# Kernel tuning notes

Measured on AMD Instinct MI355X. Metric: run time of the kernel, lower is better.

The kernel has to match this reference:

```python
import jax, jax.numpy as jnp
import numpy as np

H = 8  # num_heads
EPS = 1e-8

def setup_inputs() -> dict:
    key = jax.random.key(0)
    ks = jax.random.split(key, 8)
    B, L, E = 2, 1024, 512
    s = 1.0 / np.sqrt(E)
    return {
        "query": jax.random.normal(ks[0], (B, L, E), jnp.float32),
        "key":   jax.random.normal(ks[1], (B, L, E), jnp.float32),
        "value": jax.random.normal(ks[2], (B, L, E), jnp.float32),
        "Wq": jax.random.normal(ks[3], (E, E), jnp.float32) * s,
        "bq": jnp.zeros((E,), jnp.float32),
        "Wk": jax.random.normal(ks[4], (E, E), jnp.float32) * s,
        "bk": jnp.zeros((E,), jnp.float32),
        "Wv": jax.random.normal(ks[5], (E, E), jnp.float32) * s,
        "bv": jnp.zeros((E,), jnp.float32),
        "Wo": jax.random.normal(ks[6], (E, E), jnp.float32) * s,
        "bo": jnp.zeros((E,), jnp.float32),
    }

def reference(query, key, value, Wq, bq, Wk, bk, Wv, bv, Wo, bo):
    B, Q_len, E = query.shape
    K_len = key.shape[1]
    D = E // H
    q = (query @ Wq.T + bq).reshape(B, Q_len, H, D)
    k = (key   @ Wk.T + bk).reshape(B, K_len, H, D)
    v = (value @ Wv.T + bv).reshape(B, K_len, H, D)
    scale = 1.0 / np.sqrt(D).astype(np.float32)
    scores = jnp.einsum('bqhd,bkhd->bhqk', q, k) * scale
    # attn_norm == 'rms_head': RMS over the head axis (dim=1)
    rms = jnp.sqrt(jnp.mean(scores ** 2, axis=1, keepdims=True) + EPS)
    w = scores / rms  # [B,H,Q,K]
    # target_network == 'mlp_silu': head-summed value mix, silu, mix again
    x = jnp.einsum('bhqk,bkhd->bqkd', w, v)   # [B,Q,K,D]
    x = jax.nn.silu(x)
    x = jnp.einsum('bhqk,bqkd->bqhd', w, x)   # [B,Q,H,D]
    x = x.reshape(B, Q_len, E)
    return x @ Wo.T + bo
```

## Files before the change

### kernel.cpp

```cpp
#include <hip/hip_runtime.h>
#include <hip/hip_bf16.h>
#include <math.h>

#define BB 2
#define LL 1024
#define EE 512
#define HH 8
#define DD 64
#define NROWS (BB*LL)
#define QT 8
#define KSPLIT 4
#define KRANGE (LL/KSPLIT)

typedef __attribute__((ext_vector_type(4))) float f32x4;
typedef __attribute__((ext_vector_type(2))) float f32x2;
typedef __attribute__((ext_vector_type(8))) short short8;

static __device__ __forceinline__ short to_bf16(float f) {
    __bf16 h = (__bf16)f;
    return __builtin_bit_cast(short, h);
}

__device__ __forceinline__ void gemm_core(const float* __restrict__ X,
                                          const float* __restrict__ W,
                                          short* As, short* Bs,
                                          int m0, int n0, f32x4 (&acc)[2][2])
{
    const int tid  = threadIdx.x;
    const int lane = tid & 63, wave = tid >> 6;
    const int wr = wave >> 1, wc = wave & 1;
    const int r = tid >> 2, cq = tid & 3;
    const float* ax = X + (size_t)(m0 + r) * EE + cq * 8;
    const float* bx = W + (size_t)(n0 + r) * EE + cq * 8;

    float a_reg[8], b_reg[8];
    #pragma unroll
    for (int j = 0; j < 8; ++j) { a_reg[j] = ax[j]; b_reg[j] = bx[j]; }

    short* apos = &As[r * 32 + ((cq ^ (r & 3)) * 8)];
    short* bpos = &Bs[r * 32 + ((cq ^ (r & 3)) * 8)];
    const int swz = ((lane >> 4) ^ (lane & 3)) * 8;

    for (int it = 0; it < 16; ++it) {
        short8 av, bv;
        #pragma unroll
        for (int j = 0; j < 8; ++j) { av[j] = to_bf16(a_reg[j]); bv[j] = to_bf16(b_reg[j]); }
        __syncthreads();
        *reinterpret_cast<short8*>(apos) = av;
        *reinterpret_cast<short8*>(bpos) = bv;
        __syncthreads();
        if (it < 15) {
            const float* axn = ax + (it + 1) * 32;
            const float* bxn = bx + (it + 1) * 32;
            #pragma unroll
            for (int j = 0; j < 8; ++j) { a_reg[j] = axn[j]; b_reg[j] = bxn[j]; }
        }
        short8 af[2], bf[2];
        #pragma unroll
        for (int mi = 0; mi < 2; ++mi) {
            int row = wr * 32 + mi * 16 + (lane & 15);
            af[mi] = *reinterpret_cast<short8*>(&As[row * 32 + swz]);
        }
        #pragma unroll
        for (int ni = 0; ni < 2; ++ni) {
            int row = wc * 32 + ni * 16 + (lane & 15);
            bf[ni] = *reinterpret_cast<short8*>(&Bs[row * 32 + swz]);
        }
        #pragma unroll
        for (int mi = 0; mi < 2; ++mi)
            #pragma unroll
            for (int ni = 0; ni < 2; ++ni)
                acc[mi][ni] = __builtin_amdgcn_mfma_f32_16x16x32_bf16(af[mi], bf[ni], acc[mi][ni], 0, 0, 0);
    }
}

__global__ __launch_bounds__(256) void qkv_gemm(const float* __restrict__ q_in,
                                                const float* __restrict__ k_in,
                                                const float* __restrict__ v_in,
                                                const float* __restrict__ Wq,
                                                const float* __restrict__ Wk,
                                                const float* __restrict__ Wv,
                                                const float* __restrict__ bq,
                                                const float* __restrict__ bk,
                                                const float* __restrict__ bv,
                                                short* __restrict__ Qo,
                                                short* __restrict__ Ko,
                                                float* __restrict__ Vo)
{
    __shared__ short As[64 * 32];
    __shared__ short Bs[64 * 32];
    const int z = blockIdx.z;
    const float* X = (z == 0) ? q_in : (z == 1) ? k_in : v_in;
    const float* W = (z == 0) ? Wq : (z == 1) ? Wk : Wv;
    const float* bias = (z == 0) ? bq : (z == 1) ? bk : bv;

    const int m0 = blockIdx.x * 64, n0 = blockIdx.y * 64;
    f32x4 acc[2][2];
    #pragma unroll
    for (int mi = 0; mi < 2; ++mi)
        #pragma unroll
        for (int ni = 0; ni < 2; ++ni) acc[mi][ni] = (f32x4){0.f,0.f,0.f,0.f};

    gemm_core(X, W, As, Bs, m0, n0, acc);

    const int tid = threadIdx.x, lane = tid & 63, wave = tid >> 6;
    const int wr = wave >> 1, wc = wave & 1;
    const int col_l = lane & 15, rowg = (lane >> 4) * 4;
    #pragma unroll
    for (int mi = 0; mi < 2; ++mi)
        #pragma unroll
        for (int ni = 0; ni < 2; ++ni) {
            int colg = n0 + wc * 32 + ni * 16 + col_l;
            float bn = bias[colg];
            #pragma unroll
            for (int rr = 0; rr < 4; ++rr) {
                int mg = m0 + wr * 32 + mi * 16 + rowg + rr;
                float v = acc[mi][ni][rr] + bn;
                if (z == 2) Vo[(size_t)mg * EE + colg] = v;
                else {
                    short* ob = z ? Ko : Qo;
                    ob[(size_t)mg * EE + colg] = to_bf16(v);
                }
            }
        }
}

__global__ __launch_bounds__(256) void gemm_f32(const float* __restrict__ X,
                                                const float* __restrict__ W,
                                                const float* __restrict__ bias,
                                                float* __restrict__ out)
{
    __shared__ short As[64 * 32];
    __shared__ short Bs[64 * 32];
    const int m0 = blockIdx.x * 64, n0 = blockIdx.y * 64;
    f32x4 acc[2][2];
    #pragma unroll
    for (int mi = 0; mi < 2; ++mi)
        #pragma unroll
        for (int ni = 0; ni < 2; ++ni) acc[mi][ni] = (f32x4){0.f,0.f,0.f,0.f};

    gemm_core(X, W, As, Bs, m0, n0, acc);

    const int tid = threadIdx.x, lane = tid & 63, wave = tid >> 6;
    const int wr = wave >> 1, wc = wave & 1;
    const int col_l = lane & 15, rowg = (lane >> 4) * 4;
    #pragma unroll
    for (int mi = 0; mi < 2; ++mi)
        #pragma unroll
        for (int ni = 0; ni < 2; ++ni) {
            int colg = n0 + wc * 32 + ni * 16 + col_l;
            float bn = bias[colg];
            #pragma unroll
            for (int rr = 0; rr < 4; ++rr) {
                int mg = m0 + wr * 32 + mi * 16 + rowg + rr;
                out[(size_t)mg * EE + colg] = acc[mi][ni][rr] + bn;
            }
        }
}

__global__ __launch_bounds__(256, 4) void attn3(const short* __restrict__ Qb,
                                                const short* __restrict__ Kb,
                                                const float* __restrict__ V,
                                                float* __restrict__ ATT)
{
    __shared__ short Qs[QT * EE];
    __shared__ float sw[64 * 68];

    const int tid = threadIdx.x, lane = tid & 63, wave = tid >> 6;

    const int fid = blockIdx.x;
    const int newid = (fid & 7) * 128 + (fid >> 3);
    const int b = newid >> 9;
    const int ksp = (newid >> 7) & 3;
    const int qpos = newid & 127;
    const int bq0 = b * LL + qpos * QT;
    const int k0base = ksp * KRANGE;

    for (int i = tid; i < QT * 64; i += 256) {
        int q = i >> 6, c = i & 63;
        short8 v = *reinterpret_cast<const short8*>(Qb + ((size_t)(bq0 + q) << 9) + c * 8);
        *reinterpret_cast<short8*>(&Qs[(q << 9) + ((c ^ q) << 3)]) = v;
    }

    f32x2 oacc[4][HH];
    #pragma unroll
    for (int qp = 0; qp < 4; ++qp)
        #pragma unroll
        for (int h = 0; h < HH; ++h) oacc[qp][h] = (f32x2){0.f, 0.f};

    const int qr = (lane & 15) & 7;
    const int kg4 = lane >> 4;

    for (int t = 0; t < KRANGE / 64; ++t) {
        const int k0 = k0base + t * 64;
        __syncthreads();

        const short* kbase = Kb + ((size_t)(b * LL + k0) << 9);
        #pragma unroll
        for (int hh = 0; hh < 2; ++hh) {
            const int h = wave + hh * 4;
            short8 bfq[2];
            #pragma unroll
            for (int kc = 0; kc < 2; ++kc) {
                int c = h * 8 + kc * 4 + kg4;
                bfq[kc] = *reinterpret_cast<const short8*>(&Qs[(qr << 9) + ((c ^ qr) << 3)]);
            }
            f32x4 acc[4];
            #pragma unroll
            for (int m = 0; m < 4; ++m) acc[m] = (f32x4){0.f,0.f,0.f,0.f};
            #pragma unroll
            for (int m = 0; m < 4; ++m) {
                const short* arow = kbase + ((size_t)(m * 16 + (lane & 15)) << 9) + (h << 6) + (kg4 << 3);
                short8 af0 = *reinterpret_cast<const short8*>(arow);
                short8 af1 = *reinterpret_cast<const short8*>(arow + 32);
                acc[m] = __builtin_amdgcn_mfma_f32_16x16x32_bf16(af0, bfq[0], acc[m], 0, 0, 0);
                acc[m] = __builtin_amdgcn_mfma_f32_16x16x32_bf16(af1, bfq[1], acc[m], 0, 0, 0);
            }
            if ((lane & 15) < 8) {
                int q = lane & 15;
                #pragma unroll
                for (int m = 0; m < 4; ++m)
                    #pragma unroll
                    for (int r = 0; r < 4; ++r) {
                        int k = m * 16 + kg4 * 4 + r;
                        sw[k * 68 + h * 8 + q] = acc[m][r] * 0.125f;
                    }
            }
        }
        __syncthreads();

        #pragma unroll
        for (int rep = 0; rep < 2; ++rep) {
            int idx = rep * 256 + tid;
            int k = idx >> 3, q = idx & 7;
            float* sp = &sw[k * 68 + q];
            float s[HH], ss = 0.f;
            #pragma unroll
            for (int h = 0; h < HH; ++h) { s[h] = sp[h * 8]; ss += s[h] * s[h]; }
            float inv = rsqrtf(ss * 0.125f + 1e-8f);
            #pragma unroll
            for (int h = 0; h < HH; ++h) sp[h * 8] = s[h] * inv;
        }
        __syncthreads();

        for (int j = 0; j < 16; ++j) {
            int kl = j * 4 + wave;
            const float* vp = V + ((size_t)(b * LL + k0 + kl) << 9) + lane;
            float vr[HH];
            #pragma unroll
            for (int h = 0; h < HH; ++h) vr[h] = vp[h * DD];
            const float* swr = &sw[kl * 68];
            f32x2 xv[4];
            #pragma unroll
            for (int qp = 0; qp < 4; ++qp) xv[qp] = (f32x2){0.f, 0.f};
            #pragma unroll
            for (int h = 0; h < HH; ++h) {
                f32x4 wa = *reinterpret_cast<const f32x4*>(&swr[h * 8]);
                f32x4 wb = *reinterpret_cast<const f32x4*>(&swr[h * 8 + 4]);
                xv[0] += (f32x2){wa[0], wa[1]} * vr[h];
                xv[1] += (f32x2){wa[2], wa[3]} * vr[h];
                xv[2] += (f32x2){wb[0], wb[1]} * vr[h];
                xv[3] += (f32x2){wb[2], wb[3]} * vr[h];
            }
            #pragma unroll
            for (int qp = 0; qp < 4; ++qp) {
                xv[qp][0] = xv[qp][0] / (1.f + __expf(-xv[qp][0]));
                xv[qp][1] = xv[qp][1] / (1.f + __expf(-xv[qp][1]));
            }
            #pragma unroll
            for (int h = 0; h < HH; ++h) {
                f32x4 wa = *reinterpret_cast<const f32x4*>(&swr[h * 8]);
                f32x4 wb = *reinterpret_cast<const f32x4*>(&swr[h * 8 + 4]);
                oacc[0][h] += (f32x2){wa[0], wa[1]} * xv[0];
                oacc[1][h] += (f32x2){wa[2], wa[3]} * xv[1];
                oacc[2][h] += (f32x2){wb[0], wb[1]} * xv[2];
                oacc[3][h] += (f32x2){wb[2], wb[3]} * xv[3];
            }
        }
    }

    float* red = sw;
    for (int q = 0; q < QT; ++q) {
        __syncthreads();
        #pragma unroll
        for (int h = 0; h < HH; ++h)
            red[(wave * HH + h) * 64 + lane] = oacc[q >> 1][h][q & 1];
        __syncthreads();
        #pragma unroll
        for (int i2 = 0; i2 < 2; ++i2) {
            int e = tid + i2 * 256;
            float sum = red[e] + red[e + 512] + red[e + 1024] + red[e + 1536];
            atomicAdd(&ATT[(size_t)(bq0 + q) * EE + e], sum);
        }
    }
}

extern "C" void kernel_launch(void* const* d_in, const int* in_sizes, int n_in,
                              void* d_out, int out_size, void* d_ws, size_t ws_size,
                              hipStream_t stream) {
    const float* query = (const float*)d_in[0];
    const float* key   = (const float*)d_in[1];
    const float* value = (const float*)d_in[2];
    const float* Wq = (const float*)d_in[3];
    const float* biasq = (const float*)d_in[4];
    const float* Wk = (const float*)d_in[5];
    const float* biask = (const float*)d_in[6];
    const float* Wv = (const float*)d_in[7];
    const float* biasv = (const float*)d_in[8];
    const float* Wo = (const float*)d_in[9];
    const float* biaso = (const float*)d_in[10];
    float* out = (float*)d_out;

    char* wsb = (char*)d_ws;
    short* Qb  = (short*)(wsb);
    short* Kb  = (short*)(wsb + (2u << 20));
    float* Vb  = (float*)(wsb + (4u << 20));
    float* ATT = (float*)(wsb + (8u << 20));

    hipMemsetAsync(ATT, 0, (size_t)NROWS * EE * sizeof(float), stream);

    dim3 gQKV(NROWS / 64, EE / 64, 3);
    qkv_gemm<<<gQKV, 256, 0, stream>>>(query, key, value, Wq, Wk, Wv,
                                       biasq, biask, biasv, Qb, Kb, Vb);

    attn3<<<dim3(NROWS / QT * KSPLIT, 1, 1), dim3(256, 1, 1), 0, stream>>>(Qb, Kb, Vb, ATT);

    gemm_f32<<<dim3(NROWS / 64, EE / 64, 1), 256, 0, stream>>>(ATT, Wo, biaso, out);
}
```

Measured before the change: 246.4 us.

## Replace atomic split-K reduction with partial buffers summed in output GEMM

The attention kernel now writes each K-split's partial result to its own buffer instead of doing atomicAdd into a zeroed accumulator. The memset is dropped, and the output projection GEMM sums the four partials while loading its A operand. The change also prefetches V rows one iteration ahead in registers, replaces the division in SiLU with a hardware reciprocal, and uses the raw rsq builtin. The cost is more workspace traffic: 16 MB of partials written and then read back, in exchange for removing atomics and the memset.

```diff
diff --git a/kernel.cpp b/kernel.cpp
--- a/kernel.cpp
+++ b/kernel.cpp
@@ -19,6 +19,11 @@
 static __device__ __forceinline__ short to_bf16(float f) {
     __bf16 h = (__bf16)f;
     return __builtin_bit_cast(short, h);
+}
+
+static __device__ __forceinline__ float fast_silu(float x) {
+    float e = __expf(-x);
+    return x * __builtin_amdgcn_rcpf(1.f + e);
 }
 
 __device__ __forceinline__ void gemm_core(const float* __restrict__ X,
@@ -125,24 +130,77 @@
         }
 }
 
-__global__ __launch_bounds__(256) void gemm_f32(const float* __restrict__ X,
-                                                const float* __restrict__ W,
-                                                const float* __restrict__ bias,
-                                                float* __restrict__ out)
+__global__ __launch_bounds__(256) void gemmO(const float* __restrict__ X0,
+                                             const float* __restrict__ X1,
+                                             const float* __restrict__ X2,
+                                             const float* __restrict__ X3,
+                                             const float* __restrict__ W,
+                                             const float* __restrict__ bias,
+                                             float* __restrict__ out)
 {
     __shared__ short As[64 * 32];
     __shared__ short Bs[64 * 32];
+    const int tid  = threadIdx.x;
+    const int lane = tid & 63, wave = tid >> 6;
+    const int wr = wave >> 1, wc = wave & 1;
     const int m0 = blockIdx.x * 64, n0 = blockIdx.y * 64;
+    const int r = tid >> 2, cq = tid & 3;
+
+    size_t xoff = (size_t)(m0 + r) * EE + cq * 8;
+    const float* bx = W + (size_t)(n0 + r) * EE + cq * 8;
+
+    float a_reg[8], b_reg[8];
+    #pragma unroll
+    for (int j = 0; j < 8; ++j) {
+        a_reg[j] = X0[xoff + j] + X1[xoff + j] + X2[xoff + j] + X3[xoff + j];
+        b_reg[j] = bx[j];
+    }
+
     f32x4 acc[2][2];
     #pragma unroll
     for (int mi = 0; mi < 2; ++mi)
         #pragma unroll
         for (int ni = 0; ni < 2; ++ni) acc[mi][ni] = (f32x4){0.f,0.f,0.f,0.f};
 
-    gemm_core(X, W, As, Bs, m0, n0, acc);
-
-    const int tid = threadIdx.x, lane = tid & 63, wave = tid >> 6;
-    const int wr = wave >> 1, wc = wave & 1;
+    short* apos = &As[r * 32 + ((cq ^ (r & 3)) * 8)];
+    short* bpos = &Bs[r * 32 + ((cq ^ (r & 3)) * 8)];
+    const int swz = ((lane >> 4) ^ (lane & 3)) * 8;
+
+    for (int it = 0; it < 16; ++it) {
+        short8 av, bv;
+        #pragma unroll
+        for (int j = 0; j < 8; ++j) { av[j] = to_bf16(a_reg[j]); bv[j] = to_bf16(b_reg[j]); }
+        __syncthreads();
+        *reinterpret_cast<short8*>(apos) = av;
+        *reinterpret_cast<short8*>(bpos) = bv;
+        __syncthreads();
+        if (it < 15) {
+            size_t xo = xoff + (it + 1) * 32;
+            const float* bxn = bx + (it + 1) * 32;
+            #pragma unroll
+            for (int j = 0; j < 8; ++j) {
+                a_reg[j] = X0[xo + j] + X1[xo + j] + X2[xo + j] + X3[xo + j];
+                b_reg[j] = bxn[j];
+            }
+        }
+        short8 af[2], bf[2];
+        #pragma unroll
+        for (int mi = 0; mi < 2; ++mi) {
+            int row = wr * 32 + mi * 16 + (lane & 15);
+            af[mi] = *reinterpret_cast<short8*>(&As[row * 32 + swz]);
+        }
+        #pragma unroll
+        for (int ni = 0; ni < 2; ++ni) {
+            int row = wc * 32 + ni * 16 + (lane & 15);
+            bf[ni] = *reinterpret_cast<short8*>(&Bs[row * 32 + swz]);
+        }
+        #pragma unroll
+        for (int mi = 0; mi < 2; ++mi)
+            #pragma unroll
+            for (int ni = 0; ni < 2; ++ni)
+                acc[mi][ni] = __builtin_amdgcn_mfma_f32_16x16x32_bf16(af[mi], bf[ni], acc[mi][ni], 0, 0, 0);
+    }
+
     const int col_l = lane & 15, rowg = (lane >> 4) * 4;
     #pragma unroll
     for (int mi = 0; mi < 2; ++mi)
@@ -158,10 +216,10 @@
         }
 }
 
-__global__ __launch_bounds__(256, 4) void attn3(const short* __restrict__ Qb,
+__global__ __launch_bounds__(256, 4) void attn4(const short* __restrict__ Qb,
                                                 const short* __restrict__ Kb,
                                                 const float* __restrict__ V,
-                                                float* __restrict__ ATT)
+                                                float* __restrict__ ATTp)
 {
     __shared__ short Qs[QT * EE];
     __shared__ float sw[64 * 68];
@@ -188,11 +246,20 @@
         #pragma unroll
         for (int h = 0; h < HH; ++h) oacc[qp][h] = (f32x2){0.f, 0.f};
 
-    const int qr = (lane & 15) & 7;
+    const int qr = lane & 7;
     const int kg4 = lane >> 4;
 
     for (int t = 0; t < KRANGE / 64; ++t) {
         const int k0 = k0base + t * 64;
+        const float* vb = V + ((size_t)(b * LL + k0) << 9) + lane;
+
+        float vcur[HH];
+        {
+            const float* vp = vb + ((size_t)wave << 9);
+            #pragma unroll
+            for (int h = 0; h < HH; ++h) vcur[h] = vp[h * DD];
+        }
+
         __syncthreads();
 
         const short* kbase = Kb + ((size_t)(b * LL + k0) << 9);
@@ -237,18 +304,21 @@
             float s[HH], ss = 0.f;
             #pragma unroll
             for (int h = 0; h < HH; ++h) { s[h] = sp[h * 8]; ss += s[h] * s[h]; }
-            float inv = rsqrtf(ss * 0.125f + 1e-8f);
+            float inv = __builtin_amdgcn_rsqf(ss * 0.125f + 1e-8f);
             #pragma unroll
             for (int h = 0; h < HH; ++h) sp[h * 8] = s[h] * inv;
         }
         __syncthreads();
 
+        #pragma unroll
         for (int j = 0; j < 16; ++j) {
-            int kl = j * 4 + wave;
-            const float* vp = V + ((size_t)(b * LL + k0 + kl) << 9) + lane;
-            float vr[HH];
-            #pragma unroll
-            for (int h = 0; h < HH; ++h) vr[h] = vp[h * DD];
+            const int kl = j * 4 + wave;
+            float vnxt[HH];
+            if (j < 15) {
+                const float* vp = vb + ((size_t)(kl + 4) << 9);
+                #pragma unroll
+                for (int h = 0; h < HH; ++h) vnxt[h] = vp[h * DD];
+            }
             const float* swr = &sw[kl * 68];
             f32x2 xv[4];
             #pragma unroll
@@ -257,15 +327,15 @@
             for (int h = 0; h < HH; ++h) {
                 f32x4 wa = *reinterpret_cast<const f32x4*>(&swr[h * 8]);
                 f32x4 wb = *reinterpret_cast<const f32x4*>(&swr[h * 8 + 4]);
-                xv[0] += (f32x2){wa[0], wa[1]} * vr[h];
-                xv[1] += (f32x2){wa[2], wa[3]} * vr[h];
-                xv[2] += (f32x2){wb[0], wb[1]} * vr[h];
-                xv[3] += (f32x2){wb[2], wb[3]} * vr[h];
+                xv[0] += (f32x2){wa[0], wa[1]} * vcur[h];
+                xv[1] += (f32x2){wa[2], wa[3]} * vcur[h];
+                xv[2] += (f32x2){wb[0], wb[1]} * vcur[h];
+                xv[3] += (f32x2){wb[2], wb[3]} * vcur[h];
             }
             #pragma unroll
             for (int qp = 0; qp < 4; ++qp) {
-                xv[qp][0] = xv[qp][0] / (1.f + __expf(-xv[qp][0]));
-                xv[qp][1] = xv[qp][1] / (1.f + __expf(-xv[qp][1]));
+                xv[qp][0] = fast_silu(xv[qp][0]);
+                xv[qp][1] = fast_silu(xv[qp][1]);
             }
             #pragma unroll
             for (int h = 0; h < HH; ++h) {
@@ -276,21 +346,30 @@
                 oacc[2][h] += (f32x2){wb[0], wb[1]} * xv[2];
                 oacc[3][h] += (f32x2){wb[2], wb[3]} * xv[3];
             }
+            if (j < 15) {
+                #pragma unroll
+                for (int h = 0; h < HH; ++h) vcur[h] = vnxt[h];
+            }
         }
     }
 
     float* red = sw;
-    for (int q = 0; q < QT; ++q) {
-        __syncthreads();
-        #pragma unroll
-        for (int h = 0; h < HH; ++h)
-            red[(wave * HH + h) * 64 + lane] = oacc[q >> 1][h][q & 1];
-        __syncthreads();
-        #pragma unroll
-        for (int i2 = 0; i2 < 2; ++i2) {
-            int e = tid + i2 * 256;
-            float sum = red[e] + red[e + 512] + red[e + 1024] + red[e + 1536];
-            atomicAdd(&ATT[(size_t)(bq0 + q) * EE + e], sum);
+    float* outp = ATTp + ((size_t)ksp * NROWS + bq0) * EE;
+    for (int qq = 0; qq < 4; ++qq) {
+        __syncthreads();
+        #pragma unroll
+        for (int q2 = 0; q2 < 2; ++q2)
+            #pragma unroll
+            for (int h = 0; h < HH; ++h)
+                red[q2 * 2048 + wave * 512 + h * 64 + lane] = oacc[qq][h][q2];
+        __syncthreads();
+        #pragma unroll
+        for (int i2 = 0; i2 < 4; ++i2) {
+            int idx = i2 * 256 + tid;
+            int q2 = idx >> 9, e = idx & 511;
+            int base = q2 * 2048 + e;
+            float s = red[base] + red[base + 512] + red[base + 1024] + red[base + 1536];
+            outp[(size_t)(qq * 2 + q2) * EE + e] = s;
         }
     }
 }
@@ -315,15 +394,16 @@
     short* Qb  = (short*)(wsb);
     short* Kb  = (short*)(wsb + (2u << 20));
     float* Vb  = (float*)(wsb + (4u << 20));
-    float* ATT = (float*)(wsb + (8u << 20));
-
-    hipMemsetAsync(ATT, 0, (size_t)NROWS * EE * sizeof(float), stream);
+    float* ATTp = (float*)(wsb + (8u << 20));
+
+    const size_t PSZ = (size_t)NROWS * EE;
 
     dim3 gQKV(NROWS / 64, EE / 64, 3);
     qkv_gemm<<<gQKV, 256, 0, stream>>>(query, key, value, Wq, Wk, Wv,
                                        biasq, biask, biasv, Qb, Kb, Vb);
 
-    attn3<<<dim3(NROWS / QT * KSPLIT, 1, 1), dim3(256, 1, 1), 0, stream>>>(Qb, Kb, Vb, ATT);
-
-    gemm_f32<<<dim3(NROWS / 64, EE / 64, 1), 256, 0, stream>>>(ATT, Wo, biaso, out);
-}
+    attn4<<<dim3(NROWS / QT * KSPLIT, 1, 1), dim3(256, 1, 1), 0, stream>>>(Qb, Kb, Vb, ATTp);
+
+    gemmO<<<dim3(NROWS / 64, EE / 64, 1), 256, 0, stream>>>(ATTp, ATTp + PSZ, ATTp + 2 * PSZ, ATTp + 3 * PSZ,
+                                                            Wo, biaso, out);
+}
```

After: 427.5 us. +73.5%, slower.
